# Kernel optimization log

Hardware: AMD Instinct MI355X
Metric: run time of the kernel (lower is better)

## Reference

```python
import jax, jax.numpy as jnp
import numpy as np


def _knn(coords, k):
    # coords: [N, 3]. Returns indices of the k nearest neighbors (self excluded): [N, k]
    sq = jnp.sum(coords * coords, axis=1)
    d2 = sq[:, None] + sq[None, :] - 2.0 * (coords @ coords.T)  # [N, N]
    n = coords.shape[0]
    d2 = jnp.where(jnp.eye(n, dtype=bool), jnp.inf, d2)  # loop=False: no self edges
    _, idx = jax.lax.top_k(-d2, k)
    return idx


def setup_inputs() -> dict:
    key = jax.random.key(0)
    ks = jax.random.split(key, 7)
    B, N, C = 8, 4096, 6
    feats = jax.random.normal(ks[0], (B, N, C), dtype=jnp.float32)
    # Glorot-ish scaled weights; PyG GCNConv lin has no bias, bias added post-aggregation.
    W1 = jax.random.normal(ks[1], (6, 64), dtype=jnp.float32) * (1.0 / np.sqrt(6))
    b1 = jnp.zeros((64,), dtype=jnp.float32)
    W2 = jax.random.normal(ks[2], (64, 128), dtype=jnp.float32) * (1.0 / np.sqrt(64))
    b2 = jnp.zeros((128,), dtype=jnp.float32)
    Wf = jax.random.normal(ks[3], (128, 128), dtype=jnp.float32) * (1.0 / np.sqrt(128))
    bf = jnp.zeros((128,), dtype=jnp.float32)
    return {"feats": feats, "W1": W1, "b1": b1, "W2": W2, "b2": b2,
            "Wf": Wf, "bf": bf, "k": 16}


def reference(feats, W1, b1, W2, b2, Wf, bf, k):
    # feats: [B, N, C]; coords = first 3 channels.
    coords = feats[..., :3]
    nbr = jax.vmap(lambda c: _knn(c, k))(coords)  # [B, N, k]
    inv_deg = 1.0 / (k + 1)  # every node has exactly k in-edges + self loop (uniform sym norm)
    x = feats
    for W, b in ((W1, b1), (W2, b2)):
        h = x @ W  # [B, N, H]
        nb = jax.vmap(lambda hb, ib: hb[ib])(h, nbr)  # gather neighbor feats: [B, N, k, H]
        x = jax.nn.relu((nb.sum(axis=2) + h) * inv_deg + b)  # GCN aggregate + bias + ReLU
    return x @ Wf + bf  # [B, N, out_dim]
```

## Files before the change

### kernel.cpp

```cpp
#include <hip/hip_runtime.h>
#include <cstdint>
#include <cstddef>

#define NPTS 4096
#define KNN  16
#define INV_DEG (1.0f / 17.0f)
#define CAP  48
#define TS   512

typedef unsigned long long u64;
typedef unsigned int u32;
typedef float v2f __attribute__((ext_vector_type(2)));

#define UNUSED_K 0x7F800000FFFFFFFFull
#define SELF_K   0x7F800000FFFFFFFEull

__device__ __forceinline__ double as_f64(u64 k) { return __longlong_as_double((long long)k); }

__global__ __launch_bounds__(512) void knn_kernel(const float* __restrict__ feats,
                                                  const float* __restrict__ W1,
                                                  const float* __restrict__ b1,
                                                  int* __restrict__ nbr,
                                                  float* __restrict__ x1) {
#pragma clang fp contract(off)
  __shared__ float4 sc[TS];
  __shared__ u64 sbuf[8][2][64];

  const int b = blockIdx.x >> 8;
  const int pbase = (blockIdx.x & 255) * 16;
  const float* fb = feats + (size_t)b * NPTS * 6;
  const int wave = threadIdx.x >> 6;
  const int lane = threadIdx.x & 63;

  int ip[2];
  float xi[2], yi[2], zi[2], sqi[2], tau[2];
  u64 slot[2];
  int cnt[2];
#pragma unroll
  for (int p = 0; p < 2; ++p) {
    ip[p] = pbase + wave * 2 + p;
    const float* fr = fb + (size_t)ip[p] * 6;
    xi[p] = fr[0]; yi[p] = fr[1]; zi[p] = fr[2];
    sqi[p] = __fadd_rn(__fadd_rn(__fmul_rn(xi[p], xi[p]), __fmul_rn(yi[p], yi[p])),
                       __fmul_rn(zi[p], zi[p]));
    tau[p] = __uint_as_float(0x7f800000u);
    slot[p] = UNUSED_K;
    cnt[p] = 0;
  }

  auto flush = [&](int p) {
    u64* wb = &sbuf[wave][p][0];
    if (lane >= cnt[p] && lane < CAP) wb[lane] = UNUSED_K;
    if (lane < KNN) wb[CAP + lane] = slot[p];
    u64 myk = wb[lane];
    if ((u32)myk == (u32)ip[p]) {
      myk = SELF_K;
      wb[lane] = SELF_K;
    }
    const double dm = as_f64(myk);
    int rank = 0;
#pragma unroll
    for (int m = 0; m < 64; m += 4) {
      const double k0 = as_f64(wb[m]), k1 = as_f64(wb[m + 1]);
      const double k2 = as_f64(wb[m + 2]), k3 = as_f64(wb[m + 3]);
      rank += (int)(k0 < dm) + (int)(k1 < dm) + (int)(k2 < dm) + (int)(k3 < dm);
    }
    if (rank < KNN) wb[rank] = myk;
    u64 s15 = wb[15];
    if (lane < KNN) slot[p] = wb[lane];
    tau[p] = __uint_as_float((u32)(s15 >> 32));
    cnt[p] = 0;
  };

  for (int tb = 0; tb < NPTS; tb += TS) {
    __syncthreads();
    for (int t = threadIdx.x; t < TS; t += 512) {
      const float* fr = fb + (size_t)(tb + t) * 6;
      const float x = fr[0], y = fr[1], z = fr[2];
      const float sq = __fadd_rn(__fadd_rn(__fmul_rn(x, x), __fmul_rn(y, y)),
                                 __fmul_rn(z, z));
      float4 c; c.x = x; c.y = y; c.z = z; c.w = sq;
      sc[t] = c;
    }
    __syncthreads();

    for (int jb0 = 0; jb0 < TS; jb0 += 64) {
      const int tl = jb0 + lane;
      const int j = tb + tl;
      const float4 c = sc[tl];
      const v2f cx2 = {c.x, c.x}, cy2 = {c.y, c.y}, cz2 = {c.z, c.z},
                sq2 = {c.w, c.w};
      v2f X = {xi[0], xi[1]};
      v2f Y = {yi[0], yi[1]};
      v2f Z = {zi[0], zi[1]};
      v2f SQ = {sqi[0], sqi[1]};
      v2f dot = X * cx2;
      dot = __builtin_elementwise_fma(Y, cy2, dot);
      dot = __builtin_elementwise_fma(Z, cz2, dot);
      v2f two = {2.0f, 2.0f};
      v2f d2v = (SQ + sq2) - two * dot;
      float d2s[2] = {d2v.x, d2v.y};
#pragma unroll
      for (int p = 0; p < 2; ++p) {
        const bool pred = d2s[p] <= tau[p];
        const u64 bal = __ballot(pred);
        if (bal) {
          const int npass = __popcll(bal);
          if (cnt[p] + npass > CAP) flush(p);
          const int pos = cnt[p] + (int)__builtin_amdgcn_mbcnt_hi(
                                        (u32)(bal >> 32),
                                        __builtin_amdgcn_mbcnt_lo((u32)bal, 0));
          const u64 key = ((u64)__float_as_uint(d2s[p]) << 32) | (u32)j;
          if (npass <= CAP) {
            if (pred) sbuf[wave][p][pos] = key;
            cnt[p] += npass;
          } else {
            if (pred && pos < CAP) sbuf[wave][p][pos] = key;
            cnt[p] = CAP;
            flush(p);
            if (pred && pos >= CAP) sbuf[wave][p][pos - CAP] = key;
            cnt[p] = npass - CAP;
          }
        }
      }
    }
  }
#pragma unroll
  for (int p = 0; p < 2; ++p) flush(p);

  float* fsc = (float*)&sbuf[wave][0][0];
  float w1r[6];
#pragma unroll
  for (int k = 0; k < 6; ++k) w1r[k] = W1[k * 64 + lane];
  const float b1r = b1[lane];

#pragma unroll
  for (int p = 0; p < 2; ++p) {
    const int n = b * NPTS + ip[p];
    const int row = (lane < KNN) ? (int)(u32)slot[p] : ip[p];
    if (lane < KNN)
      nbr[(size_t)n * KNN + lane] = row;
    if (lane < 17) {
      const float* fr = fb + (size_t)row * 6;
      float2 r0 = *(const float2*)(fr);
      float2 r1 = *(const float2*)(fr + 2);
      float2 r2 = *(const float2*)(fr + 4);
      fsc[lane * 6 + 0] = r0.x; fsc[lane * 6 + 1] = r0.y;
      fsc[lane * 6 + 2] = r1.x; fsc[lane * 6 + 3] = r1.y;
      fsc[lane * 6 + 4] = r2.x; fsc[lane * 6 + 5] = r2.y;
    }
    __syncthreads();
    if (lane < 6) {
      float s = 0.f;
#pragma unroll
      for (int t = 0; t < 17; ++t) s += fsc[t * 6 + lane];
      fsc[102 + lane] = s;
    }
    __syncthreads();
    float s = 0.f;
#pragma unroll
    for (int k = 0; k < 6; ++k) s = fmaf(fsc[102 + k], w1r[k], s);
    x1[(size_t)n * 64 + lane] = fmaxf(fmaf(s, INV_DEG, b1r), 0.f);
    __syncthreads();
  }
}

__global__ __launch_bounds__(256) void enc23_kernel(const float* __restrict__ x1,
                                                    const int* __restrict__ nbr,
                                                    const float* __restrict__ W2,
                                                    const float* __restrict__ b2,
                                                    const float* __restrict__ Wf,
                                                    const float* __restrict__ bf,
                                                    float* __restrict__ out) {
  __shared__ float a1s[16][64];
  __shared__ v2f wt[16][64];
  __shared__ float xs[16][128];
  const int tid = threadIdx.x;
  const int n0 = blockIdx.x * 16;
  const int gb = n0 & ~(NPTS - 1);
  const int wave = tid >> 6, lane = tid & 63;

  {
    const int p = tid >> 4, c4 = tid & 15;
    const int n = n0 + p;
    const int* nb = nbr + (size_t)n * KNN;
    float4 s = ((const float4*)(x1 + (size_t)n * 64))[c4];
#pragma unroll
    for (int t = 0; t < KNN; ++t) {
      float4 v = ((const float4*)(x1 + (size_t)(gb + nb[t]) * 64))[c4];
      s.x += v.x; s.y += v.y; s.z += v.z; s.w += v.w;
    }
    *((float4*)&a1s[p][c4 * 4]) = s;
  }

  const int p0 = wave * 4;
  const float bx = b2[lane], by = b2[lane + 64];

  v2f acc[4];
#pragma unroll
  for (int i = 0; i < 4; ++i) acc[i] = (v2f){0, 0};
  for (int kt = 0; kt < 64; kt += 16) {
    __syncthreads();
#pragma unroll
    for (int i = 0; i < 4; ++i) {
      const int e = tid + 256 * i;
      const int k = e >> 6, l = e & 63;
      v2f w;
      w.x = W2[(kt + k) * 128 + l];
      w.y = W2[(kt + k) * 128 + 64 + l];
      wt[k][l] = w;
    }
    __syncthreads();
    for (int kk = 0; kk < 16; kk += 4) {
      float4 a[4];
#pragma unroll
      for (int i = 0; i < 4; ++i) a[i] = *(const float4*)&a1s[p0 + i][kt + kk];
#pragma unroll
      for (int j = 0; j < 4; ++j) {
        const v2f w = wt[kk + j][lane];
#pragma unroll
        for (int i = 0; i < 4; ++i) {
          const float e = j == 0 ? a[i].x : j == 1 ? a[i].y : j == 2 ? a[i].z
                                                                     : a[i].w;
          v2f v = {e, e};
          acc[i] = __builtin_elementwise_fma(v, w, acc[i]);
        }
      }
    }
  }
#pragma unroll
  for (int pi = 0; pi < 4; ++pi) {
    xs[p0 + pi][lane] = fmaxf(fmaf(acc[pi].x, INV_DEG, bx), 0.f);
    xs[p0 + pi][lane + 64] = fmaxf(fmaf(acc[pi].y, INV_DEG, by), 0.f);
  }

  v2f facc[4];
#pragma unroll
  for (int i = 0; i < 4; ++i) facc[i] = (v2f){0, 0};
  for (int jt = 0; jt < 128; jt += 16) {
    __syncthreads();
#pragma unroll
    for (int i = 0; i < 4; ++i) {
      const int e = tid + 256 * i;
      const int j = e >> 6, l = e & 63;
      v2f w;
      w.x = Wf[(jt + j) * 128 + l];
      w.y = Wf[(jt + j) * 128 + 64 + l];
      wt[j][l] = w;
    }
    __syncthreads();
    for (int jj = 0; jj < 16; jj += 4) {
      float4 a[4];
#pragma unroll
      for (int i = 0; i < 4; ++i) a[i] = *(const float4*)&xs[p0 + i][jt + jj];
#pragma unroll
      for (int j2 = 0; j2 < 4; ++j2) {
        const v2f w = wt[jj + j2][lane];
#pragma unroll
        for (int i = 0; i < 4; ++i) {
          const float e = j2 == 0 ? a[i].x : j2 == 1 ? a[i].y : j2 == 2 ? a[i].z
                                                                        : a[i].w;
          v2f v = {e, e};
          facc[i] = __builtin_elementwise_fma(v, w, facc[i]);
        }
      }
    }
  }
  const float fx = bf[lane], fy = bf[lane + 64];
#pragma unroll
  for (int pi = 0; pi < 4; ++pi) {
    float* row = out + (size_t)(n0 + p0 + pi) * 128;
    row[lane] = facc[pi].x + fx;
    row[lane + 64] = facc[pi].y + fy;
  }
}

extern "C" void kernel_launch(void* const* d_in, const int* in_sizes, int n_in,
                              void* d_out, int out_size, void* d_ws, size_t ws_size,
                              hipStream_t stream) {
  const float* feats = (const float*)d_in[0];
  const float* W1 = (const float*)d_in[1];
  const float* b1 = (const float*)d_in[2];
  const float* W2 = (const float*)d_in[3];
  const float* b2 = (const float*)d_in[4];
  const float* Wf = (const float*)d_in[5];
  const float* bf = (const float*)d_in[6];
  float* out = (float*)d_out;

  char* ws = (char*)d_ws;
  int* nbr = (int*)ws;
  float* x1 = (float*)(ws + (size_t)(2 << 20));

  knn_kernel<<<2048, 512, 0, stream>>>(feats, W1, b1, nbr, x1);
  enc23_kernel<<<2048, 256, 0, stream>>>(x1, nbr, W2, b2, Wf, bf, out);
}
```

Before: 229.1 us.

## Morton-bin points and prune kNN candidate blocks with AABB lower bounds

Adds a per-batch binning kernel that sorts points by an 8x8x8 Morton cell, and a kernel that computes per-64-point bounding boxes. The kNN kernel then scans candidates in sorted order, starting from the query's own tile, and skips any tile or block whose box lower bound exceeds the current 16th-best distance. This replaces the brute-force all-pairs scan with a pruned search. It adds two small kernels (one with only 8 blocks) and serial dependencies, and it relies on a fixed grid range of [-5,5] that is clamped at the edges.

Measured after the change: 232.3 us. No clear change (+1.4%).

```diff
diff --git a/kernel.cpp b/kernel.cpp
--- a/kernel.cpp
+++ b/kernel.cpp
@@ -6,7 +6,6 @@
 #define KNN  16
 #define INV_DEG (1.0f / 17.0f)
 #define CAP  48
-#define TS   512
 
 typedef unsigned long long u64;
 typedef unsigned int u32;
@@ -16,21 +15,113 @@
 #define SELF_K   0x7F800000FFFFFFFEull
 
 __device__ __forceinline__ double as_f64(u64 k) { return __longlong_as_double((long long)k); }
-
-__global__ __launch_bounds__(512) void knn_kernel(const float* __restrict__ feats,
+__device__ __forceinline__ int sp3(int v) { return ((v & 4) << 4) | ((v & 2) << 2) | (v & 1); }
+
+__global__ __launch_bounds__(512) void bin_kernel(const float* __restrict__ feats,
+                                                  float4* __restrict__ sortedG) {
+  __shared__ int hist[512];
+  __shared__ int tmp[512];
+  const int b = blockIdx.x;
+  const int tid = threadIdx.x;
+  const float* fb = feats + (size_t)b * NPTS * 6;
+  hist[tid] = 0;
+  __syncthreads();
+  float px[8], py[8], pz[8];
+  int pm[8];
+#pragma unroll
+  for (int i = 0; i < 8; ++i) {
+    const int n = tid + 512 * i;
+    const float* fr = fb + (size_t)n * 6;
+    const float x = fr[0], y = fr[1], z = fr[2];
+    int cx = (int)floorf((x + 5.f) * 0.8f);
+    int cy = (int)floorf((y + 5.f) * 0.8f);
+    int cz = (int)floorf((z + 5.f) * 0.8f);
+    cx = cx < 0 ? 0 : (cx > 7 ? 7 : cx);
+    cy = cy < 0 ? 0 : (cy > 7 ? 7 : cy);
+    cz = cz < 0 ? 0 : (cz > 7 ? 7 : cz);
+    const int m = sp3(cx) | (sp3(cy) << 1) | (sp3(cz) << 2);
+    px[i] = x; py[i] = y; pz[i] = z; pm[i] = m;
+    atomicAdd(&hist[m], 1);
+  }
+  __syncthreads();
+  const int myc = hist[tid];
+  int v = myc;
+  for (int off = 1; off < 512; off <<= 1) {
+    tmp[tid] = v;
+    __syncthreads();
+    if (tid >= off) v += tmp[tid - off];
+    __syncthreads();
+  }
+  hist[tid] = v - myc;
+  __syncthreads();
+#pragma unroll
+  for (int i = 0; i < 8; ++i) {
+    const int n = tid + 512 * i;
+    const int pos = atomicAdd(&hist[pm[i]], 1);
+    float4 o; o.x = px[i]; o.y = py[i]; o.z = pz[i]; o.w = (float)n;
+    sortedG[(size_t)b * NPTS + pos] = o;
+  }
+}
+
+__global__ __launch_bounds__(64) void aabb_kernel(const float4* __restrict__ sortedG,
+                                                  float4* __restrict__ aabbLo,
+                                                  float4* __restrict__ aabbHi) {
+  const int blk = blockIdx.x;
+  const int lane = threadIdx.x;
+  const float4 c = sortedG[(size_t)blk * 64 + lane];
+  float lx = c.x, ly = c.y, lz = c.z, hx = c.x, hy = c.y, hz = c.z;
+#pragma unroll
+  for (int m = 1; m < 64; m <<= 1) {
+    lx = fminf(lx, __shfl_xor(lx, m, 64));
+    ly = fminf(ly, __shfl_xor(ly, m, 64));
+    lz = fminf(lz, __shfl_xor(lz, m, 64));
+    hx = fmaxf(hx, __shfl_xor(hx, m, 64));
+    hy = fmaxf(hy, __shfl_xor(hy, m, 64));
+    hz = fmaxf(hz, __shfl_xor(hz, m, 64));
+  }
+  if (lane == 0) {
+    float4 lo; lo.x = lx; lo.y = ly; lo.z = lz; lo.w = 0.f;
+    float4 hi; hi.x = hx; hi.y = hy; hi.z = hz; hi.w = 0.f;
+    aabbLo[blk] = lo;
+    aabbHi[blk] = hi;
+  }
+}
+
+__global__ __launch_bounds__(512) void knn_kernel(const float4* __restrict__ sortedG,
+                                                  const float4* __restrict__ aabbLo,
+                                                  const float4* __restrict__ aabbHi,
+                                                  const float* __restrict__ feats,
                                                   const float* __restrict__ W1,
                                                   const float* __restrict__ b1,
                                                   int* __restrict__ nbr,
                                                   float* __restrict__ x1) {
 #pragma clang fp contract(off)
-  __shared__ float4 sc[TS];
+  __shared__ float4 slo[64], shi[64];
+  __shared__ float4 tlo[8], thi[8];
   __shared__ u64 sbuf[8][2][64];
 
   const int b = blockIdx.x >> 8;
   const int pbase = (blockIdx.x & 255) * 16;
+  const float4* sb_ = sortedG + (size_t)b * NPTS;
   const float* fb = feats + (size_t)b * NPTS * 6;
-  const int wave = threadIdx.x >> 6;
-  const int lane = threadIdx.x & 63;
+  const int tid = threadIdx.x;
+  const int wave = tid >> 6;
+  const int lane = tid & 63;
+
+  if (tid < 64) slo[tid] = aabbLo[b * 64 + tid];
+  else if (tid < 128) shi[tid - 64] = aabbHi[b * 64 + tid - 64];
+  __syncthreads();
+  if (tid < 8) {
+    float4 lo = slo[tid * 8], hi = shi[tid * 8];
+#pragma unroll
+    for (int i = 1; i < 8; ++i) {
+      const float4 l2 = slo[tid * 8 + i], h2 = shi[tid * 8 + i];
+      lo.x = fminf(lo.x, l2.x); lo.y = fminf(lo.y, l2.y); lo.z = fminf(lo.z, l2.z);
+      hi.x = fmaxf(hi.x, h2.x); hi.y = fmaxf(hi.y, h2.y); hi.z = fmaxf(hi.z, h2.z);
+    }
+    tlo[tid] = lo; thi[tid] = hi;
+  }
+  __syncthreads();
 
   int ip[2];
   float xi[2], yi[2], zi[2], sqi[2], tau[2];
@@ -38,15 +129,21 @@
   int cnt[2];
 #pragma unroll
   for (int p = 0; p < 2; ++p) {
-    ip[p] = pbase + wave * 2 + p;
-    const float* fr = fb + (size_t)ip[p] * 6;
-    xi[p] = fr[0]; yi[p] = fr[1]; zi[p] = fr[2];
+    const int s = pbase + wave * 2 + p;
+    const float4 own = sb_[s];
+    xi[p] = own.x; yi[p] = own.y; zi[p] = own.z;
+    ip[p] = (int)own.w;
     sqi[p] = __fadd_rn(__fadd_rn(__fmul_rn(xi[p], xi[p]), __fmul_rn(yi[p], yi[p])),
                        __fmul_rn(zi[p], zi[p]));
     tau[p] = __uint_as_float(0x7f800000u);
     slot[p] = UNUSED_K;
     cnt[p] = 0;
   }
+  const int ob = (pbase + wave * 2) >> 6;
+  const int ot = ob >> 3, obr = ob & 7;
+  const float wxl = fminf(xi[0], xi[1]), wxh = fmaxf(xi[0], xi[1]);
+  const float wyl = fminf(yi[0], yi[1]), wyh = fmaxf(yi[0], yi[1]);
+  const float wzl = fminf(zi[0], zi[1]), wzh = fmaxf(zi[0], zi[1]);
 
   auto flush = [&](int p) {
     u64* wb = &sbuf[wave][p][0];
@@ -72,24 +169,28 @@
     cnt[p] = 0;
   };
 
-  for (int tb = 0; tb < NPTS; tb += TS) {
-    __syncthreads();
-    for (int t = threadIdx.x; t < TS; t += 512) {
-      const float* fr = fb + (size_t)(tb + t) * 6;
-      const float x = fr[0], y = fr[1], z = fr[2];
-      const float sq = __fadd_rn(__fadd_rn(__fmul_rn(x, x), __fmul_rn(y, y)),
-                                 __fmul_rn(z, z));
-      float4 c; c.x = x; c.y = y; c.z = z; c.w = sq;
-      sc[t] = c;
-    }
-    __syncthreads();
-
-    for (int jb0 = 0; jb0 < TS; jb0 += 64) {
-      const int tl = jb0 + lane;
-      const int j = tb + tl;
-      const float4 c = sc[tl];
-      const v2f cx2 = {c.x, c.x}, cy2 = {c.y, c.y}, cz2 = {c.z, c.z},
-                sq2 = {c.w, c.w};
+  auto boxLB = [&](float4 lo, float4 hi) -> float {
+    const float dx = fmaxf(fmaxf(lo.x - wxh, wxl - hi.x), 0.f);
+    const float dy = fmaxf(fmaxf(lo.y - wyh, wyl - hi.y), 0.f);
+    const float dz = fmaxf(fmaxf(lo.z - wzh, wzl - hi.z), 0.f);
+    return dx * dx + dy * dy + dz * dz;
+  };
+
+  auto scanTile = [&](int t) {
+    {
+      const float lim = __fmaf_rn(fmaxf(tau[0], tau[1]), 1.0001f, 1e-5f);
+      if (boxLB(tlo[t], thi[t]) > lim) return;
+    }
+#pragma unroll 1
+    for (int bt = 0; bt < 8; ++bt) {
+      const int jb = t * 8 + ((t == ot) ? ((obr + bt) & 7) : bt);
+      const float lim = __fmaf_rn(fmaxf(tau[0], tau[1]), 1.0001f, 1e-5f);
+      if (boxLB(slo[jb], shi[jb]) > lim) continue;
+      const float4 c = sb_[jb * 64 + lane];
+      const float sq = __fadd_rn(__fadd_rn(__fmul_rn(c.x, c.x), __fmul_rn(c.y, c.y)),
+                                 __fmul_rn(c.z, c.z));
+      const u32 cj = (u32)(int)c.w;
+      const v2f cx2 = {c.x, c.x}, cy2 = {c.y, c.y}, cz2 = {c.z, c.z}, sq2 = {sq, sq};
       v2f X = {xi[0], xi[1]};
       v2f Y = {yi[0], yi[1]};
       v2f Z = {zi[0], zi[1]};
@@ -110,7 +211,7 @@
           const int pos = cnt[p] + (int)__builtin_amdgcn_mbcnt_hi(
                                         (u32)(bal >> 32),
                                         __builtin_amdgcn_mbcnt_lo((u32)bal, 0));
-          const u64 key = ((u64)__float_as_uint(d2s[p]) << 32) | (u32)j;
+          const u64 key = ((u64)__float_as_uint(d2s[p]) << 32) | cj;
           if (npass <= CAP) {
             if (pred) sbuf[wave][p][pos] = key;
             cnt[p] += npass;
@@ -124,7 +225,11 @@
         }
       }
     }
-  }
+  };
+
+  for (int t = ot; t >= 0; --t) scanTile(t);
+  for (int t = ot + 1; t < 8; ++t) scanTile(t);
+
 #pragma unroll
   for (int p = 0; p < 2; ++p) flush(p);
 
@@ -290,7 +395,12 @@
   char* ws = (char*)d_ws;
   int* nbr = (int*)ws;
   float* x1 = (float*)(ws + (size_t)(2 << 20));
-
-  knn_kernel<<<2048, 512, 0, stream>>>(feats, W1, b1, nbr, x1);
+  float4* sortedG = (float4*)(ws + (size_t)(10 << 20));
+  float4* aabbLo = (float4*)(ws + (size_t)(10 << 20) + (512 << 10));
+  float4* aabbHi = (float4*)(ws + (size_t)(10 << 20) + (520 << 10));
+
+  bin_kernel<<<8, 512, 0, stream>>>(feats, sortedG);
+  aabb_kernel<<<512, 64, 0, stream>>>(sortedG, aabbLo, aabbHi);
+  knn_kernel<<<2048, 512, 0, stream>>>(sortedG, aabbLo, aabbHi, feats, W1, b1, nbr, x1);
   enc23_kernel<<<2048, 256, 0, stream>>>(x1, nbr, W2, b2, Wf, bf, out);
 }
```
